# Performance work log

Measured on AMD Instinct MI355X. Metric: run time of the kernel, lower is better.

The kernel has to match this reference:

```python
import jax, jax.numpy as jnp
import numpy as np

B, M, L, D = 4, 128, 512, 768
NEG = -1e30


def setup_inputs() -> dict:
    key = jax.random.key(0)
    k1, k2 = jax.random.split(key)
    h = jax.random.normal(k1, (B, L, D), dtype=jnp.float32)
    mention_masks = jax.random.randint(k2, (B, M, L), 0, 2, dtype=jnp.int32)
    return {"h": h, "mention_masks": mention_masks}


def reference(h, mention_masks):
    # h: [B, L, D]; mention_masks: [B, M, L] (0/1)
    # Faithful to: m = (mask == 0).float() * -1e30; (m + h).max(dim=2)
    m = (mention_masks == 0).astype(h.dtype) * NEG          # [B, M, L]
    # broadcast add then max over token dim L -> [B, M, D]
    mention_reprs = jnp.max(h[:, None, :, :] + m[:, :, :, None], axis=2)
    return mention_reprs
```

## Files before the change

kernel.cpp:

```cpp
#include <hip/hip_runtime.h>

#define BB 4
#define MM 128
#define LL 512
#define DD 768
#define NEGF (-1e30f)


typedef __attribute__((address_space(1))) const unsigned int gu32_t;
typedef __attribute__((address_space(3))) unsigned int lu32_t;

#define WAITVM(N) asm volatile("s_waitcnt vmcnt(" #N ")" ::: "memory")
#define WAITLGKM0() asm volatile("s_waitcnt lgkmcnt(0)" ::: "memory")

__global__ __launch_bounds__(1024, 4) void mention_max_kernel(
    const float* __restrict__ h, const int* __restrict__ mask,
    float* __restrict__ out)
{
    const int lane = threadIdx.x & 63;
    const int wave = threadIdx.x >> 6;
    const int dch  = blockIdx.x;
    const int mch  = blockIdx.y;
    const int b    = blockIdx.z;

    const int m0 = mch * 8;
    const int l0 = wave * 32;

    __shared__ float smem[15360];

    const int half = lane >> 5;
    const int lrow = lane & 31;
    const int* mp = mask + ((size_t)(b * MM + m0)) * LL + l0 + lrow;
    int mv0 = mp[(0 + half) * LL];
    int mv1 = mp[(2 + half) * LL];
    int mv2 = mp[(4 + half) * LL];
    int mv3 = mp[(6 + half) * LL];

    const float* growbase = h + ((size_t)(b * LL + l0)) * DD + dch * 192;
    float* sbase = smem + wave * 960;

#define ISSUE(J) do {                                                         \
        __builtin_amdgcn_global_load_lds(                                     \
            (gu32_t*)(growbase + (size_t)(J) * DD + 0 * 64 + lane),           \
            (lu32_t*)(sbase + ((J) % 5) * 192 + 0 * 64), 4, 0, 0);            \
        __builtin_amdgcn_global_load_lds(                                     \
            (gu32_t*)(growbase + (size_t)(J) * DD + 1 * 64 + lane),           \
            (lu32_t*)(sbase + ((J) % 5) * 192 + 1 * 64), 4, 0, 0);            \
        __builtin_amdgcn_global_load_lds(                                     \
            (gu32_t*)(growbase + (size_t)(J) * DD + 2 * 64 + lane),           \
            (lu32_t*)(sbase + ((J) % 5) * 192 + 2 * 64), 4, 0, 0);            \
    } while (0)

    ISSUE(0); ISSUE(1); ISSUE(2); ISSUE(3); ISSUE(4);

    unsigned wbits[8];
    { unsigned long long bl = __ballot(mv0 != 0);
      wbits[0] = __builtin_amdgcn_readfirstlane((unsigned)bl);
      wbits[1] = __builtin_amdgcn_readfirstlane((unsigned)(bl >> 32)); }
    { unsigned long long bl = __ballot(mv1 != 0);
      wbits[2] = __builtin_amdgcn_readfirstlane((unsigned)bl);
      wbits[3] = __builtin_amdgcn_readfirstlane((unsigned)(bl >> 32)); }
    { unsigned long long bl = __ballot(mv2 != 0);
      wbits[4] = __builtin_amdgcn_readfirstlane((unsigned)bl);
      wbits[5] = __builtin_amdgcn_readfirstlane((unsigned)(bl >> 32)); }
    { unsigned long long bl = __ballot(mv3 != 0);
      wbits[6] = __builtin_amdgcn_readfirstlane((unsigned)bl);
      wbits[7] = __builtin_amdgcn_readfirstlane((unsigned)(bl >> 32)); }

    float accx[8], accy[8], accz[8];
#pragma unroll
    for (int m = 0; m < 8; ++m) { accx[m] = NEGF; accy[m] = NEGF; accz[m] = NEGF; }

#define CONSUME(I) do {                                                       \
        const float* sp = sbase + ((I) % 5) * 192;                            \
        const float vx = sp[lane];                                            \
        const float vy = sp[64 + lane];                                       \
        const float vz = sp[128 + lane];                                      \
        _Pragma("unroll")                                                     \
        for (int m = 0; m < 8; ++m) {                                         \
            if ((wbits[m] >> (I)) & 1u) {                                     \
                accx[m] = fmaxf(accx[m], vx);                                 \
                accy[m] = fmaxf(accy[m], vy);                                 \
                accz[m] = fmaxf(accz[m], vz);                                 \
            }                                                                 \
        }                                                                     \
    } while (0)

#pragma unroll
    for (int i = 0; i < 27; ++i) {
        WAITVM(12);
        CONSUME(i);
        WAITLGKM0();
        ISSUE(i + 5);
    }
    WAITVM(12); CONSUME(27);
    WAITVM(9);  CONSUME(28);
    WAITVM(6);  CONSUME(29);
    WAITVM(3);  CONSUME(30);
    WAITVM(0);  CONSUME(31);
#undef CONSUME
#undef ISSUE

    __syncthreads();
    float (*red)[8][3][64] = (float (*)[8][3][64])smem;
    if (wave >= 8) {
#pragma unroll
        for (int m = 0; m < 8; ++m) {
            red[wave - 8][m][0][lane] = accx[m];
            red[wave - 8][m][1][lane] = accy[m];
            red[wave - 8][m][2][lane] = accz[m];
        }
    }
    __syncthreads();
    if (wave < 8) {
#pragma unroll
        for (int m = 0; m < 8; ++m) {
            red[wave][m][0][lane] = fmaxf(accx[m], red[wave][m][0][lane]);
            red[wave][m][1][lane] = fmaxf(accy[m], red[wave][m][1][lane]);
            red[wave][m][2][lane] = fmaxf(accz[m], red[wave][m][2][lane]);
        }
    }
    __syncthreads();

    if (threadIdx.x < 512) {
        const int m  = (int)(threadIdx.x >> 6);
        const int ln = (int)(threadIdx.x & 63);
        float vx = red[0][m][0][ln];
        float vy = red[0][m][1][ln];
        float vz = red[0][m][2][ln];
#pragma unroll
        for (int w = 1; w < 8; ++w) {
            vx = fmaxf(vx, red[w][m][0][ln]);
            vy = fmaxf(vy, red[w][m][1][ln]);
            vz = fmaxf(vz, red[w][m][2][ln]);
        }
        float* op = out + ((size_t)(b * MM + m0 + m)) * DD + dch * 192;
        op[ln]       = vx;
        op[64 + ln]  = vy;
        op[128 + ln] = vz;
    }
}

extern "C" void kernel_launch(void* const* d_in, const int* in_sizes, int n_in,
                              void* d_out, int out_size, void* d_ws, size_t ws_size,
                              hipStream_t stream) {
    const float* h    = (const float*)d_in[0];
    const int*   mask = (const int*)d_in[1];
    float*       out  = (float*)d_out;
    dim3 grid(DD / 192, MM / 8, BB);
    mention_max_kernel<<<grid, dim3(1024), 0, stream>>>(h, mask, out);
}
```

Before: 74.21 us.

## Replace LDS-staged global_load_lds ring with register-ring direct global loads

Rows of h are now loaded directly into a 12-deep register ring with inline-asm global_load_dword and explicit vmcnt waits, replacing the 5-deep LDS ring filled by global_load_lds. This removes the LDS round trip and its lgkm waits, and raises the number of loads in flight per wave from 15 to 36. In exchange it uses many more VGPRs under a 1024-thread launch bound, which could cause spills or lower occupancy. It also relies on hand-written waitcnt bookkeeping for correctness.

New measurement: 69.81 us. -5.9%, faster.

```diff
diff --git a/kernel.cpp b/kernel.cpp
--- a/kernel.cpp
+++ b/kernel.cpp
@@ -5,13 +5,6 @@
 #define LL 512
 #define DD 768
 #define NEGF (-1e30f)
-
-
-typedef __attribute__((address_space(1))) const unsigned int gu32_t;
-typedef __attribute__((address_space(3))) unsigned int lu32_t;
-
-#define WAITVM(N) asm volatile("s_waitcnt vmcnt(" #N ")" ::: "memory")
-#define WAITLGKM0() asm volatile("s_waitcnt lgkmcnt(0)" ::: "memory")
 
 __global__ __launch_bounds__(1024, 4) void mention_max_kernel(
     const float* __restrict__ h, const int* __restrict__ mask,
@@ -26,32 +19,13 @@
     const int m0 = mch * 8;
     const int l0 = wave * 32;
 
-    __shared__ float smem[15360];
-
     const int half = lane >> 5;
     const int lrow = lane & 31;
     const int* mp = mask + ((size_t)(b * MM + m0)) * LL + l0 + lrow;
-    int mv0 = mp[(0 + half) * LL];
-    int mv1 = mp[(2 + half) * LL];
-    int mv2 = mp[(4 + half) * LL];
-    int mv3 = mp[(6 + half) * LL];
-
-    const float* growbase = h + ((size_t)(b * LL + l0)) * DD + dch * 192;
-    float* sbase = smem + wave * 960;
-
-#define ISSUE(J) do {                                                         \
-        __builtin_amdgcn_global_load_lds(                                     \
-            (gu32_t*)(growbase + (size_t)(J) * DD + 0 * 64 + lane),           \
-            (lu32_t*)(sbase + ((J) % 5) * 192 + 0 * 64), 4, 0, 0);            \
-        __builtin_amdgcn_global_load_lds(                                     \
-            (gu32_t*)(growbase + (size_t)(J) * DD + 1 * 64 + lane),           \
-            (lu32_t*)(sbase + ((J) % 5) * 192 + 1 * 64), 4, 0, 0);            \
-        __builtin_amdgcn_global_load_lds(                                     \
-            (gu32_t*)(growbase + (size_t)(J) * DD + 2 * 64 + lane),           \
-            (lu32_t*)(sbase + ((J) % 5) * 192 + 2 * 64), 4, 0, 0);            \
-    } while (0)
-
-    ISSUE(0); ISSUE(1); ISSUE(2); ISSUE(3); ISSUE(4);
+    const int mv0 = mp[(0 + half) * LL];
+    const int mv1 = mp[(2 + half) * LL];
+    const int mv2 = mp[(4 + half) * LL];
+    const int mv3 = mp[(6 + half) * LL];
 
     unsigned wbits[8];
     { unsigned long long bl = __ballot(mv0 != 0);
@@ -67,15 +41,33 @@
       wbits[6] = __builtin_amdgcn_readfirstlane((unsigned)bl);
       wbits[7] = __builtin_amdgcn_readfirstlane((unsigned)(bl >> 32)); }
 
+    __builtin_amdgcn_sched_barrier(0);
+
+    const float* glane = h + ((size_t)(b * LL + l0)) * DD + dch * 192 + lane;
+
+    float sx[12], sy[12], sz[12];
+
+#define ISSUE_ROW(ROW, S) do {                                                \
+        const float* _a = glane + (size_t)(ROW) * DD;                         \
+        asm volatile("global_load_dword %0, %1, off"                          \
+                     : "=v"(sx[S]) : "v"(_a) : "memory");                     \
+        asm volatile("global_load_dword %0, %1, off offset:256"               \
+                     : "=v"(sy[S]) : "v"(_a) : "memory");                     \
+        asm volatile("global_load_dword %0, %1, off offset:512"               \
+                     : "=v"(sz[S]) : "v"(_a) : "memory");                     \
+    } while (0)
+
+#define WAITROW_(N, S)                                                        \
+    asm volatile("s_waitcnt vmcnt(" #N ")"                                    \
+                 : "+v"(sx[S]), "+v"(sy[S]), "+v"(sz[S]) :: "memory")
+#define WAITROW(N, S) WAITROW_(N, S)
+
     float accx[8], accy[8], accz[8];
 #pragma unroll
     for (int m = 0; m < 8; ++m) { accx[m] = NEGF; accy[m] = NEGF; accz[m] = NEGF; }
 
-#define CONSUME(I) do {                                                       \
-        const float* sp = sbase + ((I) % 5) * 192;                            \
-        const float vx = sp[lane];                                            \
-        const float vy = sp[64 + lane];                                       \
-        const float vz = sp[128 + lane];                                      \
+#define CONSUME(I, S) do {                                                    \
+        const float vx = sx[S], vy = sy[S], vz = sz[S];                       \
         _Pragma("unroll")                                                     \
         for (int m = 0; m < 8; ++m) {                                         \
             if ((wbits[m] >> (I)) & 1u) {                                     \
@@ -86,23 +78,29 @@
         }                                                                     \
     } while (0)
 
-#pragma unroll
-    for (int i = 0; i < 27; ++i) {
-        WAITVM(12);
-        CONSUME(i);
-        WAITLGKM0();
-        ISSUE(i + 5);
-    }
-    WAITVM(12); CONSUME(27);
-    WAITVM(9);  CONSUME(28);
-    WAITVM(6);  CONSUME(29);
-    WAITVM(3);  CONSUME(30);
-    WAITVM(0);  CONSUME(31);
+    ISSUE_ROW(0, 0);  ISSUE_ROW(1, 1);  ISSUE_ROW(2, 2);  ISSUE_ROW(3, 3);
+    ISSUE_ROW(4, 4);  ISSUE_ROW(5, 5);  ISSUE_ROW(6, 6);  ISSUE_ROW(7, 7);
+    ISSUE_ROW(8, 8);  ISSUE_ROW(9, 9);  ISSUE_ROW(10, 10); ISSUE_ROW(11, 11);
+
+#define STEP(I, S) do { WAITROW(33, S); CONSUME(I, S); ISSUE_ROW((I) + 12, S); } while (0)
+    STEP(0, 0);   STEP(1, 1);   STEP(2, 2);   STEP(3, 3);
+    STEP(4, 4);   STEP(5, 5);   STEP(6, 6);   STEP(7, 7);
+    STEP(8, 8);   STEP(9, 9);   STEP(10, 10); STEP(11, 11);
+    STEP(12, 0);  STEP(13, 1);  STEP(14, 2);  STEP(15, 3);
+    STEP(16, 4);  STEP(17, 5);  STEP(18, 6);  STEP(19, 7);
+#undef STEP
+
+#define DSTEP(I, S, N) do { WAITROW(N, S); CONSUME(I, S); } while (0)
+    DSTEP(20, 8, 33);  DSTEP(21, 9, 30);  DSTEP(22, 10, 27); DSTEP(23, 11, 24);
+    DSTEP(24, 0, 21);  DSTEP(25, 1, 18);  DSTEP(26, 2, 15);  DSTEP(27, 3, 12);
+    DSTEP(28, 4, 9);   DSTEP(29, 5, 6);   DSTEP(30, 6, 3);   DSTEP(31, 7, 0);
+#undef DSTEP
 #undef CONSUME
-#undef ISSUE
+#undef WAITROW
+#undef WAITROW_
+#undef ISSUE_ROW
 
-    __syncthreads();
-    float (*red)[8][3][64] = (float (*)[8][3][64])smem;
+    __shared__ float red[8][8][3][64];
     if (wave >= 8) {
 #pragma unroll
         for (int m = 0; m < 8; ++m) {
```
